# Optimization experiments

Measured on AMD Instinct MI355X. Metric: run time of the kernel, lower is better.

## Reference

```python
import jax, jax.numpy as jnp
import numpy as np

P = 16  # patch side

def setup_inputs() -> dict:
    key = jax.random.key(0)
    k1, k2, k3, k4, k5 = jax.random.split(key, 5)
    B, H, W_img, C = 32, 512, 512, 3
    hidden = 256
    n = (H // P) * (W_img // P)
    x = jax.random.normal(k1, (B, H, W_img, C), dtype=jnp.float32)
    W = jax.random.normal(k2, (P * P * C, hidden), dtype=jnp.float32) * 0.02
    b = jax.random.normal(k3, (hidden,), dtype=jnp.float32) * 0.02
    cls_token = jax.random.normal(k4, (B, 1, hidden), dtype=jnp.float32)
    pos_embedding = jax.random.normal(k5, (B, n + 1, hidden), dtype=jnp.float32) * 0.02
    return {"x": x, "W": W, "b": b, "cls_token": cls_token, "pos_embedding": pos_embedding}

def _patchify(x):
    # (B,H,W,C) -> (B, n, P*P*C); patch index = col + (H/P)*row, flatten order (p,p,c)
    B, H, W_img, C = x.shape
    gh, gw = H // P, W_img // P
    x = x.reshape(B, gh, P, gw, P, C)
    x = x.transpose(0, 1, 3, 2, 4, 5)  # (B, gh, gw, P, P, C)
    return x.reshape(B, gh * gw, P * P * C)

def reference(x, W, b, cls_token, pos_embedding):
    patches = _patchify(x)                       # (B, n, P*P*C)
    proj = jnp.einsum('bnd,dh->bnh', patches, W) + b  # (B, n, hidden)
    out = jnp.concatenate([cls_token, proj], axis=1) + pos_embedding  # (B, n+1, hidden)
    return out
```

## Files before the change

### kernel.cpp

```cpp
#include <hip/hip_runtime.h>

#define PSZ 16
#define BATCH 32
#define IMGH 512
#define IMGW 512
#define CH 3
#define NPATCH 1024
#define K_TOT 768
#define N_TOT 256
#define ROWSTRIDE (IMGW*CH)
#define IMGSTRIDE (IMGH*IMGW*CH)

#define BM 64
#define BN 128
#define BK 64
#define KPAD 72
#define NKIT (K_TOT/BK)

typedef __bf16 bf16_t;
typedef bf16_t bf16x8 __attribute__((ext_vector_type(8)));
typedef float f32x4 __attribute__((ext_vector_type(4)));

__global__ void prep_w(const float* __restrict__ Wsrc,
                       bf16x8* __restrict__ wfh, bf16x8* __restrict__ wfl) {
    int t = blockIdx.x * 256 + threadIdx.x;
    int lane = t & 63;
    int ks = (t >> 6) & 1;
    int rest = t >> 7;
    int kit = rest % 12;
    int bcg = rest / 12;
    int col = bcg * 16 + (lane & 15);
    int kbase = kit * 64 + ks * 32 + ((lane >> 4) << 3);
    bf16x8 h, l;
#pragma unroll
    for (int e = 0; e < 8; ++e) {
        float v = Wsrc[(size_t)(kbase + e) * N_TOT + col];
        bf16_t hh = (bf16_t)v;
        h[e] = hh;
        l[e] = (bf16_t)(v - (float)hh);
    }
    wfh[t] = h;
    wfl[t] = l;
}

__global__ void cls_add(const float* __restrict__ cls, const float* __restrict__ pos,
                        float* __restrict__ out) {
    int i = blockIdx.x * 256 + threadIdx.x;
    int b = i >> 8, h = i & 255;
    size_t o = (size_t)b * (NPATCH + 1) * N_TOT + h;
    out[o] = cls[i] + pos[o];
}

__global__ __launch_bounds__(256, 4)
void patch_gemm(const float* __restrict__ x,
                const bf16x8* __restrict__ wfh, const bf16x8* __restrict__ wfl,
                const float* __restrict__ bias, const float* __restrict__ pos,
                float* __restrict__ out) {
    __shared__ bf16_t Ah[2][BM * KPAD];
    __shared__ bf16_t Al[2][BM * KPAD];

    const int bid = blockIdx.x;
    const int t = (bid & 7) * 128 + (bid >> 3);
    const int mtile = t >> 1;
    const int ntile = t & 1;

    const int tid = threadIdx.x;
    const int lane = tid & 63;
    const int wid = tid >> 6;
    const int wr = wid >> 1, wc = wid & 1;

    const int m0 = mtile * BM;
    const int n0 = ntile * BN;

    f32x4 acc[2][4] = {};

    const int l15 = lane & 15;
    const int kgrp = (lane >> 4) << 3;
    const int bcg0 = ntile * 8 + wc * 4;

    const int rowb = tid >> 3;
    const int kl8 = (tid & 7) << 3;
    const float* srcbase[2];
#pragma unroll
    for (int i = 0; i < 2; ++i) {
        int row = rowb + 32 * i;
        int pm = m0 + row;
        int b = pm >> 10, pid = pm & 1023;
        int gr = pid >> 5, gc = pid & 31;
        srcbase[i] = x + (size_t)b * IMGSTRIDE + (gr * PSZ) * ROWSTRIDE + gc * (PSZ * CH);
    }

#define LOADA(KIT, P0, P1, P2, P3)                                        \
    {                                                                      \
        int d = (KIT) * BK + kl8;                                          \
        int prow = d / 48, poff = d % 48;                                  \
        const float* s0 = srcbase[0] + prow * ROWSTRIDE + poff;            \
        const float* s1 = srcbase[1] + prow * ROWSTRIDE + poff;            \
        P0 = *(const float4*)s0;  P1 = *(const float4*)(s0 + 4);           \
        P2 = *(const float4*)s1;  P3 = *(const float4*)(s1 + 4);           \
    }

#define CVTSTORE(BUF, P0, P1, P2, P3)                                      \
    {                                                                      \
        bf16x8 h, l;                                                       \
        h[0]=(bf16_t)P0.x; l[0]=(bf16_t)(P0.x-(float)h[0]);                \
        h[1]=(bf16_t)P0.y; l[1]=(bf16_t)(P0.y-(float)h[1]);                \
        h[2]=(bf16_t)P0.z; l[2]=(bf16_t)(P0.z-(float)h[2]);                \
        h[3]=(bf16_t)P0.w; l[3]=(bf16_t)(P0.w-(float)h[3]);                \
        h[4]=(bf16_t)P1.x; l[4]=(bf16_t)(P1.x-(float)h[4]);                \
        h[5]=(bf16_t)P1.y; l[5]=(bf16_t)(P1.y-(float)h[5]);                \
        h[6]=(bf16_t)P1.z; l[6]=(bf16_t)(P1.z-(float)h[6]);                \
        h[7]=(bf16_t)P1.w; l[7]=(bf16_t)(P1.w-(float)h[7]);                \
        *reinterpret_cast<bf16x8*>(&Ah[BUF][rowb * KPAD + kl8]) = h;       \
        *reinterpret_cast<bf16x8*>(&Al[BUF][rowb * KPAD + kl8]) = l;       \
        h[0]=(bf16_t)P2.x; l[0]=(bf16_t)(P2.x-(float)h[0]);                \
        h[1]=(bf16_t)P2.y; l[1]=(bf16_t)(P2.y-(float)h[1]);                \
        h[2]=(bf16_t)P2.z; l[2]=(bf16_t)(P2.z-(float)h[2]);                \
        h[3]=(bf16_t)P2.w; l[3]=(bf16_t)(P2.w-(float)h[3]);                \
        h[4]=(bf16_t)P3.x; l[4]=(bf16_t)(P3.x-(float)h[4]);                \
        h[5]=(bf16_t)P3.y; l[5]=(bf16_t)(P3.y-(float)h[5]);                \
        h[6]=(bf16_t)P3.z; l[6]=(bf16_t)(P3.z-(float)h[6]);                \
        h[7]=(bf16_t)P3.w; l[7]=(bf16_t)(P3.w-(float)h[7]);                \
        *reinterpret_cast<bf16x8*>(&Ah[BUF][(rowb + 32) * KPAD + kl8]) = h;\
        *reinterpret_cast<bf16x8*>(&Al[BUF][(rowb + 32) * KPAD + kl8]) = l;\
    }

    float4 p0, p1, p2, p3;
    LOADA(0, p0, p1, p2, p3);
    CVTSTORE(0, p0, p1, p2, p3);
    __syncthreads();

#pragma unroll 2
    for (int kit = 0; kit < NKIT; ++kit) {
        const int cur = kit & 1;
        if (kit < NKIT - 1) LOADA(kit + 1, p0, p1, p2, p3);

#pragma unroll
        for (int ks = 0; ks < 2; ++ks) {
            bf16x8 bfh[4], bfl[4];
#pragma unroll
            for (int bc = 0; bc < 4; ++bc) {
                int idx = (((bcg0 + bc) * 12 + kit) * 2 + ks) * 64 + lane;
                bfh[bc] = wfh[idx];
                bfl[bc] = wfl[idx];
            }
            const int kb = ks * 32 + kgrp;
            bf16x8 afh[2], afl[2];
#pragma unroll
            for (int ar = 0; ar < 2; ++ar) {
                int o = (wr * 32 + ar * 16 + l15) * KPAD + kb;
                afh[ar] = *reinterpret_cast<const bf16x8*>(&Ah[cur][o]);
                afl[ar] = *reinterpret_cast<const bf16x8*>(&Al[cur][o]);
            }
#pragma unroll
            for (int ar = 0; ar < 2; ++ar)
#pragma unroll
                for (int bc = 0; bc < 4; ++bc) {
                    acc[ar][bc] = __builtin_amdgcn_mfma_f32_16x16x32_bf16(afh[ar], bfh[bc], acc[ar][bc], 0, 0, 0);
                    acc[ar][bc] = __builtin_amdgcn_mfma_f32_16x16x32_bf16(afh[ar], bfl[bc], acc[ar][bc], 0, 0, 0);
                    acc[ar][bc] = __builtin_amdgcn_mfma_f32_16x16x32_bf16(afl[ar], bfh[bc], acc[ar][bc], 0, 0, 0);
                }
        }

        if (kit < NKIT - 1) CVTSTORE(cur ^ 1, p0, p1, p2, p3);
        __syncthreads();
    }

    const int colbase = n0 + wc * 64;
    float bvals[4];
#pragma unroll
    for (int bc = 0; bc < 4; ++bc) bvals[bc] = bias[colbase + bc * 16 + l15];

#pragma unroll
    for (int ar = 0; ar < 2; ++ar) {
        int rbase = m0 + wr * 32 + ar * 16 + ((lane >> 4) << 2);
#pragma unroll
        for (int j = 0; j < 4; ++j) {
            int pm = rbase + j;
            int b = pm >> 10, p = pm & 1023;
            size_t orow = (size_t)(b * (NPATCH + 1) + 1 + p) * N_TOT;
#pragma unroll
            for (int bc = 0; bc < 4; ++bc) {
                int col = colbase + bc * 16 + l15;
                out[orow + col] = acc[ar][bc][j] + bvals[bc] + pos[orow + col];
            }
        }
    }
#undef LOADA
#undef CVTSTORE
}

extern "C" void kernel_launch(void* const* d_in, const int* in_sizes, int n_in,
                              void* d_out, int out_size, void* d_ws, size_t ws_size,
                              hipStream_t stream) {
    const float* x    = (const float*)d_in[0];
    const float* W    = (const float*)d_in[1];
    const float* bias = (const float*)d_in[2];
    const float* cls  = (const float*)d_in[3];
    const float* pos  = (const float*)d_in[4];
    float* out = (float*)d_out;

    bf16x8* wfh = (bf16x8*)d_ws;
    bf16x8* wfl = wfh + 24576;

    prep_w<<<96, 256, 0, stream>>>(W, wfh, wfl);
    cls_add<<<32, 256, 0, stream>>>(cls, pos, out);
    patch_gemm<<<1024, 256, 0, stream>>>(x, wfh, wfl, bias, pos, out);
}
```

Measured before the change: 215.3 us.

## Stage fp32 A tiles via direct global-to-LDS loads with swizzle, convert at read

Replaces the register-staged load and bf16 hi/lo conversion of the A tile with buffer global_load_lds copies of raw fp32 data into a swizzled LDS layout. The split into high and low bf16 parts now happens after the LDS read, just before the MFMAs. B fragments are double-buffered in registers and the k loop is manually unrolled by two. Launch bounds drop to 2 blocks per CU. The aim is to remove the VGPR round trip and the LDS store instructions, at the cost of more register pressure and lower occupancy. Conversion work is also now repeated by each wave that reads the same rows.

```diff
diff --git a/kernel.cpp b/kernel.cpp
--- a/kernel.cpp
+++ b/kernel.cpp
@@ -14,8 +14,7 @@
 #define BM 64
 #define BN 128
 #define BK 64
-#define KPAD 72
-#define NKIT (K_TOT/BK)
+#define NKIT 12
 
 typedef __bf16 bf16_t;
 typedef bf16_t bf16x8 __attribute__((ext_vector_type(8)));
@@ -51,13 +50,18 @@
     out[o] = cls[i] + pos[o];
 }
 
-__global__ __launch_bounds__(256, 4)
+__device__ __forceinline__ void gload_lds16(const void* g, void* l) {
+    __builtin_amdgcn_global_load_lds(
+        (const __attribute__((address_space(1))) void*)g,
+        (__attribute__((address_space(3))) void*)l, 16, 0, 0);
+}
+
+__global__ __launch_bounds__(256, 2)
 void patch_gemm(const float* __restrict__ x,
                 const bf16x8* __restrict__ wfh, const bf16x8* __restrict__ wfl,
                 const float* __restrict__ bias, const float* __restrict__ pos,
                 float* __restrict__ out) {
-    __shared__ bf16_t Ah[2][BM * KPAD];
-    __shared__ bf16_t Al[2][BM * KPAD];
+    __shared__ float Af[2][BM * BK];
 
     const int bid = blockIdx.x;
     const int t = (bid & 7) * 128 + (bid >> 3);
@@ -75,95 +79,106 @@
     f32x4 acc[2][4] = {};
 
     const int l15 = lane & 15;
-    const int kgrp = (lane >> 4) << 3;
+    const int lg = lane >> 4;
     const int bcg0 = ntile * 8 + wc * 4;
 
-    const int rowb = tid >> 3;
-    const int kl8 = (tid & 7) << 3;
-    const float* srcbase[2];
-#pragma unroll
-    for (int i = 0; i < 2; ++i) {
-        int row = rowb + 32 * i;
-        int pm = m0 + row;
+    const float* gsrc[4];
+    int kf[4];
+#pragma unroll
+    for (int r = 0; r < 4; ++r) {
+        int R = wid * 16 + r * 4 + lg;
+        int c = l15;
+        int cp = (c & 8) | ((c & 7) ^ (R & 7));
+        kf[r] = cp << 2;
+        int pm = m0 + R;
         int b = pm >> 10, pid = pm & 1023;
         int gr = pid >> 5, gc = pid & 31;
-        srcbase[i] = x + (size_t)b * IMGSTRIDE + (gr * PSZ) * ROWSTRIDE + gc * (PSZ * CH);
-    }
-
-#define LOADA(KIT, P0, P1, P2, P3)                                        \
-    {                                                                      \
-        int d = (KIT) * BK + kl8;                                          \
-        int prow = d / 48, poff = d % 48;                                  \
-        const float* s0 = srcbase[0] + prow * ROWSTRIDE + poff;            \
-        const float* s1 = srcbase[1] + prow * ROWSTRIDE + poff;            \
-        P0 = *(const float4*)s0;  P1 = *(const float4*)(s0 + 4);           \
-        P2 = *(const float4*)s1;  P3 = *(const float4*)(s1 + 4);           \
-    }
-
-#define CVTSTORE(BUF, P0, P1, P2, P3)                                      \
-    {                                                                      \
-        bf16x8 h, l;                                                       \
-        h[0]=(bf16_t)P0.x; l[0]=(bf16_t)(P0.x-(float)h[0]);                \
-        h[1]=(bf16_t)P0.y; l[1]=(bf16_t)(P0.y-(float)h[1]);                \
-        h[2]=(bf16_t)P0.z; l[2]=(bf16_t)(P0.z-(float)h[2]);                \
-        h[3]=(bf16_t)P0.w; l[3]=(bf16_t)(P0.w-(float)h[3]);                \
-        h[4]=(bf16_t)P1.x; l[4]=(bf16_t)(P1.x-(float)h[4]);                \
-        h[5]=(bf16_t)P1.y; l[5]=(bf16_t)(P1.y-(float)h[5]);                \
-        h[6]=(bf16_t)P1.z; l[6]=(bf16_t)(P1.z-(float)h[6]);                \
-        h[7]=(bf16_t)P1.w; l[7]=(bf16_t)(P1.w-(float)h[7]);                \
-        *reinterpret_cast<bf16x8*>(&Ah[BUF][rowb * KPAD + kl8]) = h;       \
-        *reinterpret_cast<bf16x8*>(&Al[BUF][rowb * KPAD + kl8]) = l;       \
-        h[0]=(bf16_t)P2.x; l[0]=(bf16_t)(P2.x-(float)h[0]);                \
-        h[1]=(bf16_t)P2.y; l[1]=(bf16_t)(P2.y-(float)h[1]);                \
-        h[2]=(bf16_t)P2.z; l[2]=(bf16_t)(P2.z-(float)h[2]);                \
-        h[3]=(bf16_t)P2.w; l[3]=(bf16_t)(P2.w-(float)h[3]);                \
-        h[4]=(bf16_t)P3.x; l[4]=(bf16_t)(P3.x-(float)h[4]);                \
-        h[5]=(bf16_t)P3.y; l[5]=(bf16_t)(P3.y-(float)h[5]);                \
-        h[6]=(bf16_t)P3.z; l[6]=(bf16_t)(P3.z-(float)h[6]);                \
-        h[7]=(bf16_t)P3.w; l[7]=(bf16_t)(P3.w-(float)h[7]);                \
-        *reinterpret_cast<bf16x8*>(&Ah[BUF][(rowb + 32) * KPAD + kl8]) = h;\
-        *reinterpret_cast<bf16x8*>(&Al[BUF][(rowb + 32) * KPAD + kl8]) = l;\
-    }
-
-    float4 p0, p1, p2, p3;
-    LOADA(0, p0, p1, p2, p3);
-    CVTSTORE(0, p0, p1, p2, p3);
+        gsrc[r] = x + (size_t)b * IMGSTRIDE + (gr * PSZ) * ROWSTRIDE + gc * (PSZ * CH);
+    }
+
+    int rdoff[2][2];
+#pragma unroll
+    for (int ks = 0; ks < 2; ++ks)
+#pragma unroll
+        for (int ar = 0; ar < 2; ++ar) {
+            int R = wr * 32 + ar * 16 + l15;
+            int c0 = ks * 8 + ((lg * 2) ^ (l15 & 7));
+            rdoff[ks][ar] = R * 256 + c0 * 16;
+        }
+
+#define STAGE(KIT, BUF)                                                        \
+    {                                                                          \
+        _Pragma("unroll")                                                      \
+        for (int r = 0; r < 4; ++r) {                                          \
+            int d = (KIT) * BK + kf[r];                                        \
+            int prow = d / 48, poff = d - prow * 48;                           \
+            gload_lds16(gsrc[r] + prow * ROWSTRIDE + poff,                     \
+                        &Af[BUF][(wid * 16 + r * 4) * BK]);                    \
+        }                                                                      \
+    }
+
+#define LOADB(KIT, BH, BL)                                                     \
+    {                                                                          \
+        _Pragma("unroll")                                                      \
+        for (int ks = 0; ks < 2; ++ks)                                         \
+            _Pragma("unroll")                                                  \
+            for (int bc = 0; bc < 4; ++bc) {                                   \
+                int idx = (((bcg0 + bc) * 12 + (KIT)) * 2 + ks) * 64 + lane;   \
+                BH[ks][bc] = wfh[idx];                                         \
+                BL[ks][bc] = wfl[idx];                                         \
+            }                                                                  \
+    }
+
+#define COMPUTE(BUF, BH, BL)                                                   \
+    {                                                                          \
+        _Pragma("unroll")                                                      \
+        for (int ks = 0; ks < 2; ++ks)                                         \
+            _Pragma("unroll")                                                  \
+            for (int ar = 0; ar < 2; ++ar) {                                   \
+                const char* base = (const char*)&Af[BUF][0];                   \
+                f32x4 f0 = *(const f32x4*)(base + rdoff[ks][ar]);              \
+                f32x4 f1 = *(const f32x4*)(base + (rdoff[ks][ar] ^ 16));       \
+                bf16x8 ah, al;                                                 \
+                ah[0]=(bf16_t)f0[0]; al[0]=(bf16_t)(f0[0]-(float)ah[0]);       \
+                ah[1]=(bf16_t)f0[1]; al[1]=(bf16_t)(f0[1]-(float)ah[1]);       \
+                ah[2]=(bf16_t)f0[2]; al[2]=(bf16_t)(f0[2]-(float)ah[2]);       \
+                ah[3]=(bf16_t)f0[3]; al[3]=(bf16_t)(f0[3]-(float)ah[3]);       \
+                ah[4]=(bf16_t)f1[0]; al[4]=(bf16_t)(f1[0]-(float)ah[4]);       \
+                ah[5]=(bf16_t)f1[1]; al[5]=(bf16_t)(f1[1]-(float)ah[5]);       \
+                ah[6]=(bf16_t)f1[2]; al[6]=(bf16_t)(f1[2]-(float)ah[6]);       \
+                ah[7]=(bf16_t)f1[3]; al[7]=(bf16_t)(f1[3]-(float)ah[7]);       \
+                _Pragma("unroll")                                              \
+                for (int bc = 0; bc < 4; ++bc) {                               \
+                    acc[ar][bc] = __builtin_amdgcn_mfma_f32_16x16x32_bf16(ah, BH[ks][bc], acc[ar][bc], 0, 0, 0); \
+                    acc[ar][bc] = __builtin_amdgcn_mfma_f32_16x16x32_bf16(ah, BL[ks][bc], acc[ar][bc], 0, 0, 0); \
+                    acc[ar][bc] = __builtin_amdgcn_mfma_f32_16x16x32_bf16(al, BH[ks][bc], acc[ar][bc], 0, 0, 0); \
+                }                                                              \
+            }                                                                  \
+    }
+
+    bf16x8 B0h[2][4], B0l[2][4], B1h[2][4], B1l[2][4];
+
+    STAGE(0, 0);
+    LOADB(0, B0h, B0l);
     __syncthreads();
 
-#pragma unroll 2
-    for (int kit = 0; kit < NKIT; ++kit) {
-        const int cur = kit & 1;
-        if (kit < NKIT - 1) LOADA(kit + 1, p0, p1, p2, p3);
-
-#pragma unroll
-        for (int ks = 0; ks < 2; ++ks) {
-            bf16x8 bfh[4], bfl[4];
-#pragma unroll
-            for (int bc = 0; bc < 4; ++bc) {
-                int idx = (((bcg0 + bc) * 12 + kit) * 2 + ks) * 64 + lane;
-                bfh[bc] = wfh[idx];
-                bfl[bc] = wfl[idx];
+    for (int kp = 0; kp < 6; ++kp) {
+        {
+            const int kit = 2 * kp;
+            STAGE(kit + 1, 1);
+            LOADB(kit + 1, B1h, B1l);
+            COMPUTE(0, B0h, B0l);
+            __syncthreads();
+        }
+        {
+            const int kit = 2 * kp + 1;
+            if (kp < 5) {
+                STAGE(kit + 1, 0);
+                LOADB(kit + 1, B0h, B0l);
             }
-            const int kb = ks * 32 + kgrp;
-            bf16x8 afh[2], afl[2];
-#pragma unroll
-            for (int ar = 0; ar < 2; ++ar) {
-                int o = (wr * 32 + ar * 16 + l15) * KPAD + kb;
-                afh[ar] = *reinterpret_cast<const bf16x8*>(&Ah[cur][o]);
-                afl[ar] = *reinterpret_cast<const bf16x8*>(&Al[cur][o]);
-            }
-#pragma unroll
-            for (int ar = 0; ar < 2; ++ar)
-#pragma unroll
-                for (int bc = 0; bc < 4; ++bc) {
-                    acc[ar][bc] = __builtin_amdgcn_mfma_f32_16x16x32_bf16(afh[ar], bfh[bc], acc[ar][bc], 0, 0, 0);
-                    acc[ar][bc] = __builtin_amdgcn_mfma_f32_16x16x32_bf16(afh[ar], bfl[bc], acc[ar][bc], 0, 0, 0);
-                    acc[ar][bc] = __builtin_amdgcn_mfma_f32_16x16x32_bf16(afl[ar], bfh[bc], acc[ar][bc], 0, 0, 0);
-                }
-        }
-
-        if (kit < NKIT - 1) CVTSTORE(cur ^ 1, p0, p1, p2, p3);
-        __syncthreads();
+            COMPUTE(1, B1h, B1l);
+            __syncthreads();
+        }
     }
 
     const int colbase = n0 + wc * 64;
@@ -173,7 +188,7 @@
 
 #pragma unroll
     for (int ar = 0; ar < 2; ++ar) {
-        int rbase = m0 + wr * 32 + ar * 16 + ((lane >> 4) << 2);
+        int rbase = m0 + wr * 32 + ar * 16 + (lg << 2);
 #pragma unroll
         for (int j = 0; j < 4; ++j) {
             int pm = rbase + j;
@@ -186,8 +201,9 @@
             }
         }
     }
-#undef LOADA
-#undef CVTSTORE
+#undef STAGE
+#undef LOADB
+#undef COMPUTE
 }
 
 extern "C" void kernel_launch(void* const* d_in, const int* in_sizes, int n_in,
```

After: 212.0 us. No clear change (-1.5%).
